# Performance work log

Hardware: AMD Instinct MI355X
Metric: run time of the kernel (lower is better)

The kernel has to match this reference:

```python
import jax, jax.numpy as jnp
import numpy as np

LOSS_WEIGHT = 1.0  # init kwarg, reduction='mean'


def setup_inputs() -> dict:
    key = jax.random.key(0)
    k1, k2 = jax.random.split(key)
    C, N = 128, 1024
    x = jax.random.normal(k1, (C, N), dtype=jnp.float32)
    soft_target = jax.random.normal(k2, (C, N), dtype=jnp.float32)
    return {"x": x, "soft_target": soft_target}


def _relation(f):
    # matrix1[c,i,j] = f[c,j]; matrix2[c,i,j] = f[c,i]
    # relation[c,i,j] = (f[c,j] - f[c,i])**2  -> [C, N, N]
    d = f[:, None, :] - f[:, :, None]
    return d * d


def reference(x, soft_target):
    rel_s = _relation(x)             # [C, N, N]
    rel_t = _relation(soft_target)   # [C, N, N]
    diff = rel_s - rel_t
    # F.mse_loss default reduction='mean'; outer @weighted_loss 'mean' on a
    # scalar is a no-op, so the result is loss_weight * mean((rel_s-rel_t)^2).
    return LOSS_WEIGHT * jnp.mean(diff * diff)
```

## Files before the change

### kernel.cpp

```cpp
#include <hip/hip_runtime.h>


#define C_CH 128
#define N_EL 1024
#define NS 12

__global__ __launch_bounds__(256) void relloss_stage1(
    const float* __restrict__ x, const float* __restrict__ t,
    double* __restrict__ ws) {
  const int c = blockIdx.x;
  const int tid = threadIdx.x;
  const float* __restrict__ xr = x + c * N_EL;
  const float* __restrict__ tr = t + c * N_EL;

  double s[NS];
#pragma unroll
  for (int k = 0; k < NS; ++k) s[k] = 0.0;

  for (int i = tid; i < N_EL; i += 256) {
    const double xv = (double)xr[i];
    const double tv = (double)tr[i];
    const double x2 = xv * xv, t2 = tv * tv;
    s[0] += xv;
    s[1] += x2;
    s[2] += x2 * xv;
    s[3] += x2 * x2;
    s[4] += tv;
    s[5] += t2;
    s[6] += t2 * tv;
    s[7] += t2 * t2;
    s[8] += xv * tv;
    s[9] += x2 * tv;
    s[10] += xv * t2;
    s[11] += x2 * t2;
  }

#pragma unroll
  for (int k = 0; k < NS; ++k) {
#pragma unroll
    for (int off = 32; off > 0; off >>= 1) s[k] += __shfl_down(s[k], off, 64);
  }

  __shared__ double lds[4][NS];
  const int wave = tid >> 6;
  const int lane = tid & 63;
  if (lane == 0) {
#pragma unroll
    for (int k = 0; k < NS; ++k) lds[wave][k] = s[k];
  }
  __syncthreads();

  if (tid == 0) {
    double r[NS];
#pragma unroll
    for (int k = 0; k < NS; ++k)
      r[k] = lds[0][k] + lds[1][k] + lds[2][k] + lds[3][k];
    const double Nn = (double)N_EL;
    const double termX = 2.0 * Nn * r[3] - 8.0 * r[2] * r[0] + 6.0 * r[1] * r[1];
    const double termT = 2.0 * Nn * r[7] - 8.0 * r[6] * r[4] + 6.0 * r[5] * r[5];
    const double cross = 2.0 * Nn * r[11] - 4.0 * r[9] * r[4] - 4.0 * r[10] * r[0] +
                         2.0 * r[1] * r[5] + 4.0 * r[8] * r[8];
    ws[c] = termX - 2.0 * cross + termT;
  }
}

__global__ __launch_bounds__(128) void relloss_stage2(
    const double* __restrict__ ws, float* __restrict__ out) {
  const int tid = threadIdx.x;
  double v = ws[tid];
#pragma unroll
  for (int off = 32; off > 0; off >>= 1) v += __shfl_down(v, off, 64);
  __shared__ double lds[2];
  if ((tid & 63) == 0) lds[tid >> 6] = v;
  __syncthreads();
  if (tid == 0) {
    const double total = lds[0] + lds[1];
    out[0] = (float)(total / ((double)C_CH * (double)N_EL * (double)N_EL));
  }
}

extern "C" void kernel_launch(void* const* d_in, const int* in_sizes, int n_in,
                              void* d_out, int out_size, void* d_ws, size_t ws_size,
                              hipStream_t stream) {
  const float* x = (const float*)d_in[0];
  const float* t = (const float*)d_in[1];
  double* ws = (double*)d_ws;
  float* out = (float*)d_out;

  relloss_stage1<<<C_CH, 256, 0, stream>>>(x, t, ws);
  relloss_stage2<<<1, 128, 0, stream>>>(ws, out);
}
```

Baseline: 10.78 us.

## Fuse two reduction stages via atomic last-block counter, single-wave blocks

Merges the per-channel moment kernel and the final reduction kernel into one launch, where the last block to finish (found with an atomic counter) sums the per-channel terms. Each block becomes a single 64-lane wave using float4 loads, which removes the LDS cross-wave step and the __syncthreads. A hipMemsetAsync is added to reset the counter on each call, so there is still an extra stream operation, now a memset in place of the second kernel launch.

Result: slower. 16.60 us (+54.1%).

```diff
diff --git a/kernel.cpp b/kernel.cpp
--- a/kernel.cpp
+++ b/kernel.cpp
@@ -3,80 +3,72 @@
 
 #define C_CH 128
 #define N_EL 1024
-#define NS 12
 
-__global__ __launch_bounds__(256) void relloss_stage1(
+__global__ __launch_bounds__(64) void relloss_fused(
     const float* __restrict__ x, const float* __restrict__ t,
-    double* __restrict__ ws) {
+    double* __restrict__ ws, unsigned int* __restrict__ counter,
+    float* __restrict__ out) {
   const int c = blockIdx.x;
-  const int tid = threadIdx.x;
-  const float* __restrict__ xr = x + c * N_EL;
-  const float* __restrict__ tr = t + c * N_EL;
+  const int lane = threadIdx.x;
 
-  double s[NS];
+  const float4* __restrict__ x4 = (const float4*)(x + c * N_EL);
+  const float4* __restrict__ t4 = (const float4*)(t + c * N_EL);
+
+  double s1x = 0, s2x = 0, s3x = 0, s4x = 0;
+  double s1t = 0, s2t = 0, s3t = 0, s4t = 0;
+  double sxt = 0, sx2t = 0, sxt2 = 0, sx2t2 = 0;
+
 #pragma unroll
-  for (int k = 0; k < NS; ++k) s[k] = 0.0;
-
-  for (int i = tid; i < N_EL; i += 256) {
-    const double xv = (double)xr[i];
-    const double tv = (double)tr[i];
-    const double x2 = xv * xv, t2 = tv * tv;
-    s[0] += xv;
-    s[1] += x2;
-    s[2] += x2 * xv;
-    s[3] += x2 * x2;
-    s[4] += tv;
-    s[5] += t2;
-    s[6] += t2 * tv;
-    s[7] += t2 * t2;
-    s[8] += xv * tv;
-    s[9] += x2 * tv;
-    s[10] += xv * t2;
-    s[11] += x2 * t2;
+  for (int it = 0; it < 4; ++it) {
+    const float4 xv4 = x4[lane + it * 64];
+    const float4 tv4 = t4[lane + it * 64];
+    const float xs[4] = {xv4.x, xv4.y, xv4.z, xv4.w};
+    const float ts[4] = {tv4.x, tv4.y, tv4.z, tv4.w};
+#pragma unroll
+    for (int j = 0; j < 4; ++j) {
+      const double xv = (double)xs[j];
+      const double tv = (double)ts[j];
+      const double x2 = xv * xv, t2 = tv * tv;
+      s1x += xv;  s2x += x2;  s3x += x2 * xv;  s4x += x2 * x2;
+      s1t += tv;  s2t += t2;  s3t += t2 * tv;  s4t += t2 * t2;
+      sxt += xv * tv;  sx2t += x2 * tv;  sxt2 += xv * t2;  sx2t2 += x2 * t2;
+    }
   }
 
-#pragma unroll
-  for (int k = 0; k < NS; ++k) {
-#pragma unroll
-    for (int off = 32; off > 0; off >>= 1) s[k] += __shfl_down(s[k], off, 64);
+#define WRED(v)                                        \
+  _Pragma("unroll")                                    \
+  for (int o = 32; o > 0; o >>= 1) (v) += __shfl_down((v), (o), 64);
+
+  WRED(s1x) WRED(s2x) WRED(s3x) WRED(s4x)
+  WRED(s1t) WRED(s2t) WRED(s3t) WRED(s4t)
+  WRED(sxt) WRED(sx2t) WRED(sxt2) WRED(sx2t2)
+
+  unsigned int tk = 0;
+  if (lane == 0) {
+    const double Nn = (double)N_EL;
+    const double termX = 2.0 * Nn * s4x - 8.0 * s3x * s1x + 6.0 * s2x * s2x;
+    const double termT = 2.0 * Nn * s4t - 8.0 * s3t * s1t + 6.0 * s2t * s2t;
+    const double cross = 2.0 * Nn * sx2t2 - 4.0 * sx2t * s1t - 4.0 * sxt2 * s1x +
+                         2.0 * s2x * s2t + 4.0 * sxt * sxt;
+    const double term = termX - 2.0 * cross + termT;
+    __hip_atomic_store(&ws[c], term, __ATOMIC_RELEASE, __HIP_MEMORY_SCOPE_AGENT);
+    tk = __hip_atomic_fetch_add(counter, 1u, __ATOMIC_ACQ_REL,
+                                __HIP_MEMORY_SCOPE_AGENT);
   }
+  tk = (unsigned int)__shfl((int)tk, 0, 64);
 
-  __shared__ double lds[4][NS];
-  const int wave = tid >> 6;
-  const int lane = tid & 63;
-  if (lane == 0) {
-#pragma unroll
-    for (int k = 0; k < NS; ++k) lds[wave][k] = s[k];
+  if (tk == C_CH - 1) {
+    double a = __hip_atomic_load(&ws[lane], __ATOMIC_ACQUIRE,
+                                 __HIP_MEMORY_SCOPE_AGENT);
+    double b = __hip_atomic_load(&ws[lane + 64], __ATOMIC_ACQUIRE,
+                                 __HIP_MEMORY_SCOPE_AGENT);
+    double v = a + b;
+    WRED(v)
+    if (lane == 0) {
+      out[0] = (float)(v * 0x1p-27);
+    }
   }
-  __syncthreads();
-
-  if (tid == 0) {
-    double r[NS];
-#pragma unroll
-    for (int k = 0; k < NS; ++k)
-      r[k] = lds[0][k] + lds[1][k] + lds[2][k] + lds[3][k];
-    const double Nn = (double)N_EL;
-    const double termX = 2.0 * Nn * r[3] - 8.0 * r[2] * r[0] + 6.0 * r[1] * r[1];
-    const double termT = 2.0 * Nn * r[7] - 8.0 * r[6] * r[4] + 6.0 * r[5] * r[5];
-    const double cross = 2.0 * Nn * r[11] - 4.0 * r[9] * r[4] - 4.0 * r[10] * r[0] +
-                         2.0 * r[1] * r[5] + 4.0 * r[8] * r[8];
-    ws[c] = termX - 2.0 * cross + termT;
-  }
-}
-
-__global__ __launch_bounds__(128) void relloss_stage2(
-    const double* __restrict__ ws, float* __restrict__ out) {
-  const int tid = threadIdx.x;
-  double v = ws[tid];
-#pragma unroll
-  for (int off = 32; off > 0; off >>= 1) v += __shfl_down(v, off, 64);
-  __shared__ double lds[2];
-  if ((tid & 63) == 0) lds[tid >> 6] = v;
-  __syncthreads();
-  if (tid == 0) {
-    const double total = lds[0] + lds[1];
-    out[0] = (float)(total / ((double)C_CH * (double)N_EL * (double)N_EL));
-  }
+#undef WRED
 }
 
 extern "C" void kernel_launch(void* const* d_in, const int* in_sizes, int n_in,
@@ -85,8 +77,9 @@
   const float* x = (const float*)d_in[0];
   const float* t = (const float*)d_in[1];
   double* ws = (double*)d_ws;
+  unsigned int* counter = (unsigned int*)((char*)d_ws + C_CH * sizeof(double));
   float* out = (float*)d_out;
 
-  relloss_stage1<<<C_CH, 256, 0, stream>>>(x, t, ws);
-  relloss_stage2<<<1, 128, 0, stream>>>(ws, out);
+  hipMemsetAsync(counter, 0, sizeof(unsigned int), stream);
+  relloss_fused<<<C_CH, 64, 0, stream>>>(x, t, ws, counter, out);
 }
```
